# Kernel tuning notes

Measured on AMD Instinct MI355X. Metric: run time of the kernel, lower is better.

## Reference

```python
import jax, jax.numpy as jnp
import numpy as np

D_MODEL = 1024
N_HEADS = 16
HEAD_DIM = D_MODEL // N_HEADS  # 64
BATCH, SEQ = 2, 2048
MASK_FILL = -1000000000.0


def setup_inputs() -> dict:
    key = jax.random.key(0)
    ks = jax.random.split(key, 13)
    s = 1.0 / np.sqrt(D_MODEL)
    inp = {
        "q": jax.random.normal(ks[0], (BATCH, SEQ, D_MODEL), jnp.float32),
        "k": jax.random.normal(ks[1], (BATCH, SEQ, D_MODEL), jnp.float32),
        "v": jax.random.normal(ks[2], (BATCH, SEQ, D_MODEL), jnp.float32),
        "mask": jax.random.randint(ks[3], (BATCH, 1, SEQ, SEQ), 0, 2, jnp.int32),
        "Wq": jax.random.normal(ks[4], (D_MODEL, D_MODEL), jnp.float32) * s,
        "bq": jax.random.normal(ks[5], (D_MODEL,), jnp.float32) * s,
        "Wk": jax.random.normal(ks[6], (D_MODEL, D_MODEL), jnp.float32) * s,
        "bk": jax.random.normal(ks[7], (D_MODEL,), jnp.float32) * s,
        "Wv": jax.random.normal(ks[8], (D_MODEL, D_MODEL), jnp.float32) * s,
        "bv": jax.random.normal(ks[9], (D_MODEL,), jnp.float32) * s,
        "Wo": jax.random.normal(ks[10], (D_MODEL, D_MODEL), jnp.float32) * s,
        "bo": jax.random.normal(ks[11], (D_MODEL,), jnp.float32) * s,
    }
    return inp


def reference(q, k, v, mask, Wq, bq, Wk, bk, Wv, bv, Wo, bo):
    batch, seq, feat = q.shape
    # Linear projections (torch Linear: x @ W.T + b)
    qp = q @ Wq.T + bq
    kp = k @ Wk.T + bk
    vp = v @ Wv.T + bv

    def split(x):
        # (B, S, D) -> (B, H, S, Dh)
        return x.reshape(batch, seq, N_HEADS, HEAD_DIM).swapaxes(1, 2)

    qh, kh, vh = split(qp), split(kp), split(vp)

    # (B, H, S, S) score matrix, scaled
    score = jnp.einsum("bhqd,bhkd->bhqk", qh, kh) / jnp.sqrt(
        jnp.asarray(HEAD_DIM, qh.dtype))
    score = jnp.where(mask == 0, jnp.asarray(MASK_FILL, score.dtype), score)
    attn = jax.nn.softmax(score, axis=-1)
    out = jnp.einsum("bhqk,bhkd->bhqd", attn, vh)  # (B, H, S, Dh)
    joint = out.swapaxes(1, 2).reshape(batch, seq, feat)
    return joint @ Wo.T + bo
```

## Files before the change

kernel.cpp:

```cpp
#include <hip/hip_runtime.h>

typedef unsigned short u16;
typedef unsigned long long u64;
typedef float f32x4 __attribute__((ext_vector_type(4)));
typedef __bf16 bf16x4 __attribute__((ext_vector_type(4)));
typedef __bf16 bf16x8 __attribute__((ext_vector_type(8)));
typedef u16 u16x8 __attribute__((ext_vector_type(8)));

#define QSCALE 0.18033688011112042f

__device__ __forceinline__ u16 f2bf(float f) {
  unsigned int u = __float_as_uint(f);
  u += 0x7fffu + ((u >> 16) & 1u);
  return (u16)(u >> 16);
}

__device__ __forceinline__ void async16(const void* g, void* l) {
  __builtin_amdgcn_global_load_lds(
      (__attribute__((address_space(1))) void*)g,
      (__attribute__((address_space(3))) void*)l,
      16, 0, 0);
}

__device__ __forceinline__ f32x4 mfma16(bf16x8 a, bf16x8 b, f32x4 c) {
  return __builtin_amdgcn_mfma_f32_16x16x32_bf16(a, b, c, 0, 0, 0);
}

struct CvtArgs {
  const float* src[7];
  u16* dst[7];
};

__global__ __launch_bounds__(256) void cvt_kernel(CvtArgs a) {
  int z = blockIdx.z;
  int n = (z < 3) ? 4194304 : 1048576;
  int base = (blockIdx.x * 256 + threadIdx.x) * 8;
  if (base >= n) return;
  const float* s = a.src[z] + base;
  f32x4 x0 = *(const f32x4*)s;
  f32x4 x1 = *(const f32x4*)(s + 4);
  u16x8 pk;
  pk[0]=f2bf(x0[0]); pk[1]=f2bf(x0[1]); pk[2]=f2bf(x0[2]); pk[3]=f2bf(x0[3]);
  pk[4]=f2bf(x1[0]); pk[5]=f2bf(x1[1]); pk[6]=f2bf(x1[2]); pk[7]=f2bf(x1[3]);
  *(u16x8*)(a.dst[z] + base) = pk;
}

__global__ __launch_bounds__(256) void pack_mask_kernel(
    const int* __restrict__ mask, u64* __restrict__ pm) {
  int idx = blockIdx.x * 256 + threadIdx.x;
  const int4* src = (const int4*)(mask + (size_t)idx * 64);
  u64 bits = 0ull;
#pragma unroll
  for (int j = 0; j < 16; ++j) {
    int4 v = src[j];
    if (v.x) bits |= 1ull << (4 * j + 0);
    if (v.y) bits |= 1ull << (4 * j + 1);
    if (v.z) bits |= 1ull << (4 * j + 2);
    if (v.w) bits |= 1ull << (4 * j + 3);
  }
  pm[idx] = bits;
}

__device__ __forceinline__ void gemm_body(const u16* __restrict__ A,
                                          const u16* __restrict__ W,
                                          const float* __restrict__ bias,
                                          void* __restrict__ outraw, int mode,
                                          float oscale) {
  alignas(16) __shared__ u16 lA[128 * 32];
  alignas(16) __shared__ u16 lB[128 * 32];
  const int tid = threadIdx.x;
  const int lane = tid & 63, wv = tid >> 6;
  const int wm = wv >> 1, wn = wv & 1;
  const int m0 = blockIdx.y * 128, n0 = blockIdx.x * 128;
  const int l15 = lane & 15, quad = lane >> 4;
  const int srow = lane >> 2;
  const int scol = (lane & 3) * 8;

  f32x4 acc[4][4] = {};

  for (int k0 = 0; k0 < 1024; k0 += 32) {
#pragma unroll
    for (int t = 0; t < 2; ++t) {
      int rb = (wv * 2 + t) * 16;
      async16(A + (size_t)(m0 + rb + srow) * 1024 + k0 + scol, (char*)lA + rb * 64);
      async16(W + (size_t)(n0 + rb + srow) * 1024 + k0 + scol, (char*)lB + rb * 64);
    }
    __syncthreads();
    bf16x8 af[4], bfr[4];
#pragma unroll
    for (int i = 0; i < 4; ++i) {
      af[i]  = *(const bf16x8*)(lA + (wm * 64 + i * 16 + l15) * 32 + quad * 8);
      bfr[i] = *(const bf16x8*)(lB + (wn * 64 + i * 16 + l15) * 32 + quad * 8);
    }
#pragma unroll
    for (int i = 0; i < 4; ++i)
#pragma unroll
      for (int j = 0; j < 4; ++j)
        acc[i][j] = mfma16(af[i], bfr[j], acc[i][j]);
    __syncthreads();
  }

#pragma unroll
  for (int i = 0; i < 4; ++i) {
    int mbase = m0 + wm * 64 + i * 16 + quad * 4;
#pragma unroll
    for (int j = 0; j < 4; ++j) {
      int n = n0 + wn * 64 + j * 16 + l15;
      float bv = bias[n];
#pragma unroll
      for (int r = 0; r < 4; ++r) {
        int m = mbase + r;
        float val = (acc[i][j][r] + bv) * oscale;
        if (mode == 0) {
          int b = m >> 11, s = m & 2047, h = n >> 6, dh = n & 63;
          ((u16*)outraw)[((((size_t)b * 16 + h) * 2048 + s) << 6) + dh] = f2bf(val);
        } else if (mode == 1) {
          int b = m >> 11, s = m & 2047, h = n >> 6, dh = n & 63;
          ((u16*)outraw)[((((size_t)b * 16 + h) * 64 + dh) << 11) + s] = f2bf(val);
        } else {
          ((float*)outraw)[(size_t)m * 1024 + n] = val;
        }
      }
    }
  }
}

__global__ __launch_bounds__(256) void gemm_qkv_kernel(
    const u16* __restrict__ qb, const u16* __restrict__ kb, const u16* __restrict__ vb,
    const u16* __restrict__ Wqb, const float* __restrict__ bq,
    const u16* __restrict__ Wkb, const float* __restrict__ bk,
    const u16* __restrict__ Wvb, const float* __restrict__ bv,
    u16* __restrict__ qp, u16* __restrict__ kp, u16* __restrict__ vt) {
  if (blockIdx.z == 0)      gemm_body(qb, Wqb, bq, qp, 0, QSCALE);
  else if (blockIdx.z == 1) gemm_body(kb, Wkb, bk, kp, 0, 1.0f);
  else                      gemm_body(vb, Wvb, bv, vt, 1, 1.0f);
}

__global__ __launch_bounds__(256) void gemm_o_kernel(
    const u16* __restrict__ joint, const u16* __restrict__ Wob,
    const float* __restrict__ bo, float* __restrict__ out) {
  gemm_body(joint, Wob, bo, out, 2, 1.0f);
}

__global__ __launch_bounds__(256, 4) void attn_kernel(
    const u16* __restrict__ qp, const u16* __restrict__ kp,
    const u16* __restrict__ vt, const u64* __restrict__ pm,
    u16* __restrict__ joint) {
  alignas(16) __shared__ u16 kbuf[2][4096];
  alignas(16) __shared__ u16 vbuf[2][4096];
  alignas(16) __shared__ u16 pbuf[4][1024];

  const int tid = threadIdx.x, lane = tid & 63, wv = tid >> 6;
  const int quad = lane >> 4, l15 = lane & 15;
  const int q0 = blockIdx.x * 64;
  const int h = blockIdx.y, b = blockIdx.z;
  const size_t head_off = ((size_t)b * 16 + h) * 2048 * 64;
  const u16* Qh = qp + head_off;
  const u16* Kh = kp + head_off;
  const u16* Vh = vt + head_off;
  const int qr = q0 + wv * 16 + l15;
  const u64* pmq = pm + ((size_t)b * 2048 + qr) * 32;

  bf16x8 qf[2];
  {
    const u16* qrow = Qh + (size_t)qr * 64 + quad * 8;
    qf[0] = *(const bf16x8*)(qrow);
    qf[1] = *(const bf16x8*)(qrow + 32);
  }

  const int sd0 = tid, sd1 = 256 + tid;
  const int snt0 = sd0 >> 7, shalf0 = (sd0 >> 6) & 1, sl60 = sd0 & 63;
  const int snt1 = sd1 >> 7, shalf1 = (sd1 >> 6) & 1, sl61 = sd1 & 63;
  const u16* kg0 = Kh + (size_t)(snt0 * 16 + (sl60 & 15)) * 64 + shalf0 * 32 + (sl60 >> 4) * 8;
  const u16* kg1 = Kh + (size_t)(snt1 * 16 + (sl61 & 15)) * 64 + shalf1 * 32 + (sl61 >> 4) * 8;
  const int vb0 = sd0 >> 6, vb1 = sd1 >> 6;
  const u16* vg0 = Vh + (size_t)((vb0 >> 1) * 16 + (sl60 & 15)) * 2048 + (vb0 & 1) * 32 + (sl60 >> 4) * 8;
  const u16* vg1 = Vh + (size_t)((vb1 >> 1) * 16 + (sl61 & 15)) * 2048 + (vb1 & 1) * 32 + (sl61 >> 4) * 8;

  f32x4 O[4] = {};
  f32x4 lacc = {};
  const f32x4 fz = {};

  async16(kg0, (char*)kbuf[0] + sd0 * 16);
  async16(kg1, (char*)kbuf[0] + sd1 * 16);
  async16(vg0, (char*)vbuf[0] + sd0 * 16);
  async16(vg1, (char*)vbuf[0] + sd1 * 16);

  for (int kt = 0; kt < 32; ++kt) {
    __syncthreads();

    if (kt != 31) {
      const size_t kadv = (size_t)(kt + 1) * 4096;
      const int vadv = (kt + 1) * 64;
      char* kd = (char*)kbuf[(kt + 1) & 1];
      char* vd = (char*)vbuf[(kt + 1) & 1];
      async16(kg0 + kadv, kd + sd0 * 16);
      async16(kg1 + kadv, kd + sd1 * 16);
      async16(vg0 + vadv, vd + sd0 * 16);
      async16(vg1 + vadv, vd + sd1 * 16);
    }

    u64 word = pmq[kt];
    const u16* kc = kbuf[kt & 1];
    const u16* vc = vbuf[kt & 1];

    bf16x8 kf[8];
#pragma unroll
    for (int nt = 0; nt < 4; ++nt) {
      kf[2 * nt]     = *(const bf16x8*)(kc + nt * 1024 + lane * 8);
      kf[2 * nt + 1] = *(const bf16x8*)(kc + nt * 1024 + 512 + lane * 8);
    }

    f32x4 S[4];
#pragma unroll
    for (int nt = 0; nt < 4; ++nt) {
      f32x4 z = mfma16(kf[2 * nt], qf[0], fz);
      S[nt] = mfma16(kf[2 * nt + 1], qf[1], z);
    }

    {
      unsigned int wlo = (unsigned int)word, whi = (unsigned int)(word >> 32);
#pragma unroll
      for (int nt = 0; nt < 4; ++nt) {
        unsigned int hw = (nt < 2) ? wlo : whi;
        unsigned int nib = hw >> ((nt & 1) * 16 + quad * 4);
#pragma unroll
        for (int r = 0; r < 4; ++r) {
          float pe = __builtin_amdgcn_exp2f(S[nt][r]);
          S[nt][r] = ((nib >> r) & 1u) ? pe : 0.f;
        }
        lacc += S[nt];
        bf16x4 pv = __builtin_convertvector(S[nt], bf16x4);
        int t4 = 4 * nt + quad;
        int ks = t4 >> 3, qd = (t4 & 7) >> 1;
        u16* pw = pbuf[wv] + ks * 512 + qd * 128 + l15 * 8 + (t4 & 1) * 4;
        *(u64*)pw = *(const u64*)&pv;
      }
    }

    bf16x8 vf[8];
#pragma unroll
    for (int nt = 0; nt < 4; ++nt) {
      vf[2 * nt]     = *(const bf16x8*)(vc + (nt * 2) * 512 + lane * 8);
      vf[2 * nt + 1] = *(const bf16x8*)(vc + (nt * 2 + 1) * 512 + lane * 8);
    }
    asm volatile("s_waitcnt lgkmcnt(0)" ::: "memory");

#pragma unroll
    for (int ks = 0; ks < 2; ++ks) {
      bf16x8 pf = *(const bf16x8*)(pbuf[wv] + ks * 512 + lane * 8);
#pragma unroll
      for (int nt = 0; nt < 4; ++nt)
        O[nt] = mfma16(vf[2 * nt + ks], pf, O[nt]);
    }
  }

  {
    float l = (lacc[0] + lacc[1]) + (lacc[2] + lacc[3]);
    l += __shfl_xor(l, 16, 64);
    l += __shfl_xor(l, 32, 64);
    float inv = 1.0f / l;
    size_t row_off = ((size_t)b * 2048 + qr) * 1024 + h * 64;
#pragma unroll
    for (int nt = 0; nt < 4; ++nt) {
      f32x4 ov = O[nt] * inv;
      bf16x4 obv = __builtin_convertvector(ov, bf16x4);
      *(u64*)(joint + row_off + nt * 16 + quad * 4) = *(const u64*)&obv;
    }
  }
}

extern "C" void kernel_launch(void* const* d_in, const int* in_sizes, int n_in,
                              void* d_out, int out_size, void* d_ws, size_t ws_size,
                              hipStream_t stream) {
  const float* q  = (const float*)d_in[0];
  const float* k  = (const float*)d_in[1];
  const float* v  = (const float*)d_in[2];
  const int* mask = (const int*)d_in[3];
  const float* Wq = (const float*)d_in[4];
  const float* bq = (const float*)d_in[5];
  const float* Wk = (const float*)d_in[6];
  const float* bk = (const float*)d_in[7];
  const float* Wv = (const float*)d_in[8];
  const float* bv = (const float*)d_in[9];
  const float* Wo = (const float*)d_in[10];
  const float* bo = (const float*)d_in[11];
  float* out = (float*)d_out;

  u16* w = (u16*)d_ws;
  u16* qp    = w;
  u16* kp    = w + 4194304;
  u16* vt    = w + 8388608;
  u16* qb    = w + 12582912;
  u16* kb    = w + 16777216;
  u16* vb    = w + 20971520;
  u16* Wqb   = w + 25165824;
  u16* Wkb   = w + 26214400;
  u16* Wvb   = w + 27262976;
  u16* Wob   = w + 28311552;
  u64* pm    = (u64*)(w + 29360128);
  u16* joint = qb;

  CvtArgs ca;
  ca.src[0] = q;  ca.dst[0] = qb;
  ca.src[1] = k;  ca.dst[1] = kb;
  ca.src[2] = v;  ca.dst[2] = vb;
  ca.src[3] = Wq; ca.dst[3] = Wqb;
  ca.src[4] = Wk; ca.dst[4] = Wkb;
  ca.src[5] = Wv; ca.dst[5] = Wvb;
  ca.src[6] = Wo; ca.dst[6] = Wob;

  pack_mask_kernel<<<dim3(512), dim3(256), 0, stream>>>(mask, pm);
  cvt_kernel<<<dim3(2048, 1, 7), dim3(256), 0, stream>>>(ca);
  gemm_qkv_kernel<<<dim3(8, 32, 3), dim3(256), 0, stream>>>(
      qb, kb, vb, Wqb, bq, Wkb, bk, Wvb, bv, qp, kp, vt);
  attn_kernel<<<dim3(32, 16, 2), dim3(256), 0, stream>>>(qp, kp, vt, pm, joint);
  gemm_o_kernel<<<dim3(8, 32, 1), dim3(256), 0, stream>>>(joint, Wob, bo, out);
}
```

Measured before the change: 300.4 us.

## Rewrite attention with 32x32 MFMA, register-resident P and swizzled LDS

The attention kernel moves from 16x16x32 to 32x32x16 bf16 MFMA tiles, so each wave handles 32 query rows and each block handles 128 queries, halving the grid. Instead of staging P through a per-wave LDS buffer, the probabilities are packed to bf16 in registers and rearranged across lanes with permlane32 swaps to form the B operand directly. K/V tiles are loaded into LDS with an XOR swizzle to avoid bank conflicts. This removes the P round trip through LDS and its waitcnt, but it raises register pressure (launch bounds drop to 2 blocks per SM) and gives fewer blocks to spread across CUs.

```diff
diff --git a/kernel.cpp b/kernel.cpp
--- a/kernel.cpp
+++ b/kernel.cpp
@@ -1,11 +1,14 @@
 #include <hip/hip_runtime.h>
 
 typedef unsigned short u16;
+typedef unsigned int u32;
 typedef unsigned long long u64;
 typedef float f32x4 __attribute__((ext_vector_type(4)));
+typedef float f32x16 __attribute__((ext_vector_type(16)));
 typedef __bf16 bf16x4 __attribute__((ext_vector_type(4)));
 typedef __bf16 bf16x8 __attribute__((ext_vector_type(8)));
 typedef u16 u16x8 __attribute__((ext_vector_type(8)));
+typedef u32 u32x4 __attribute__((ext_vector_type(4)));
 
 #define QSCALE 0.18033688011112042f
 
@@ -24,6 +27,20 @@
 
 __device__ __forceinline__ f32x4 mfma16(bf16x8 a, bf16x8 b, f32x4 c) {
   return __builtin_amdgcn_mfma_f32_16x16x32_bf16(a, b, c, 0, 0, 0);
+}
+
+__device__ __forceinline__ f32x16 mfma32(bf16x8 a, bf16x8 b, f32x16 c) {
+  return __builtin_amdgcn_mfma_f32_32x32x16_bf16(a, b, c, 0, 0, 0);
+}
+
+__device__ __forceinline__ u32 cvtpk(float lo, float hi) {
+  u32 r;
+  asm("v_cvt_pk_bf16_f32 %0, %1, %2" : "=v"(r) : "v"(lo), "v"(hi));
+  return r;
+}
+
+__device__ __forceinline__ void pswap(u32& a, u32& b) {
+  asm("v_permlane32_swap_b32 %0, %1" : "+v"(a), "+v"(b));
 }
 
 struct CvtArgs {
@@ -142,44 +159,42 @@
   gemm_body(joint, Wob, bo, out, 2, 1.0f);
 }
 
-__global__ __launch_bounds__(256, 4) void attn_kernel(
+__global__ __launch_bounds__(256, 2) void attn_kernel(
     const u16* __restrict__ qp, const u16* __restrict__ kp,
     const u16* __restrict__ vt, const u64* __restrict__ pm,
     u16* __restrict__ joint) {
   alignas(16) __shared__ u16 kbuf[2][4096];
   alignas(16) __shared__ u16 vbuf[2][4096];
-  alignas(16) __shared__ u16 pbuf[4][1024];
 
   const int tid = threadIdx.x, lane = tid & 63, wv = tid >> 6;
-  const int quad = lane >> 4, l15 = lane & 15;
-  const int q0 = blockIdx.x * 64;
-  const int h = blockIdx.y, b = blockIdx.z;
-  const size_t head_off = ((size_t)b * 16 + h) * 2048 * 64;
+  const int l31 = lane & 31, hi = lane >> 5, l7 = lane & 7;
+  const int q0 = blockIdx.x * 128;
+  const int hd = blockIdx.y, b = blockIdx.z;
+  const size_t head_off = ((size_t)b * 16 + hd) * 2048 * 64;
   const u16* Qh = qp + head_off;
   const u16* Kh = kp + head_off;
   const u16* Vh = vt + head_off;
-  const int qr = q0 + wv * 16 + l15;
+  const int qr = q0 + wv * 32 + l31;
   const u64* pmq = pm + ((size_t)b * 2048 + qr) * 32;
 
-  bf16x8 qf[2];
+  bf16x8 qf[4];
   {
-    const u16* qrow = Qh + (size_t)qr * 64 + quad * 8;
-    qf[0] = *(const bf16x8*)(qrow);
-    qf[1] = *(const bf16x8*)(qrow + 32);
+    const u16* qrow = Qh + (size_t)qr * 64 + hi * 8;
+#pragma unroll
+    for (int d = 0; d < 4; ++d) qf[d] = *(const bf16x8*)(qrow + d * 16);
   }
 
   const int sd0 = tid, sd1 = 256 + tid;
-  const int snt0 = sd0 >> 7, shalf0 = (sd0 >> 6) & 1, sl60 = sd0 & 63;
-  const int snt1 = sd1 >> 7, shalf1 = (sd1 >> 6) & 1, sl61 = sd1 & 63;
-  const u16* kg0 = Kh + (size_t)(snt0 * 16 + (sl60 & 15)) * 64 + shalf0 * 32 + (sl60 >> 4) * 8;
-  const u16* kg1 = Kh + (size_t)(snt1 * 16 + (sl61 & 15)) * 64 + shalf1 * 32 + (sl61 >> 4) * 8;
-  const int vb0 = sd0 >> 6, vb1 = sd1 >> 6;
-  const u16* vg0 = Vh + (size_t)((vb0 >> 1) * 16 + (sl60 & 15)) * 2048 + (vb0 & 1) * 32 + (sl60 >> 4) * 8;
-  const u16* vg1 = Vh + (size_t)((vb1 >> 1) * 16 + (sl61 & 15)) * 2048 + (vb1 & 1) * 32 + (sl61 >> 4) * 8;
-
-  f32x4 O[4] = {};
+  const int kr0 = sd0 >> 3, ks0 = ((sd0 & 7) ^ (kr0 & 7)) * 8;
+  const int kr1 = sd1 >> 3, ks1 = ((sd1 & 7) ^ (kr1 & 7)) * 8;
+  const u16* kg0 = Kh + (size_t)kr0 * 64 + ks0;
+  const u16* kg1 = Kh + (size_t)kr1 * 64 + ks1;
+  const u16* vg0 = Vh + (size_t)kr0 * 2048 + ks0;
+  const u16* vg1 = Vh + (size_t)kr1 * 2048 + ks1;
+
+  f32x16 O[2] = {};
   f32x4 lacc = {};
-  const f32x4 fz = {};
+  const f32x16 fz16 = {};
 
   async16(kg0, (char*)kbuf[0] + sd0 * 16);
   async16(kg1, (char*)kbuf[0] + sd1 * 16);
@@ -201,72 +216,95 @@
     }
 
     u64 word = pmq[kt];
-    const u16* kc = kbuf[kt & 1];
-    const u16* vc = vbuf[kt & 1];
-
-    bf16x8 kf[8];
-#pragma unroll
-    for (int nt = 0; nt < 4; ++nt) {
-      kf[2 * nt]     = *(const bf16x8*)(kc + nt * 1024 + lane * 8);
-      kf[2 * nt + 1] = *(const bf16x8*)(kc + nt * 1024 + 512 + lane * 8);
-    }
-
-    f32x4 S[4];
-#pragma unroll
-    for (int nt = 0; nt < 4; ++nt) {
-      f32x4 z = mfma16(kf[2 * nt], qf[0], fz);
-      S[nt] = mfma16(kf[2 * nt + 1], qf[1], z);
-    }
+    const char* kc = (const char*)kbuf[kt & 1];
+    const char* vc = (const char*)vbuf[kt & 1];
+
+    bf16x8 kf[2][4];
+#pragma unroll
+    for (int h = 0; h < 2; ++h)
+#pragma unroll
+      for (int d = 0; d < 4; ++d)
+        kf[h][d] = *(const bf16x8*)(kc + (h * 32 + l31) * 128 +
+                                    (((2 * d + hi) ^ l7) << 4));
+
+    f32x16 S[2];
+#pragma unroll
+    for (int h = 0; h < 2; ++h) {
+      f32x16 s = mfma32(kf[h][0], qf[0], fz16);
+      s = mfma32(kf[h][1], qf[1], s);
+      s = mfma32(kf[h][2], qf[2], s);
+      S[h] = mfma32(kf[h][3], qf[3], s);
+    }
+
+    bf16x8 vf[2][4];
+#pragma unroll
+    for (int g = 0; g < 2; ++g)
+#pragma unroll
+      for (int ks = 0; ks < 4; ++ks)
+        vf[g][ks] = *(const bf16x8*)(vc + (g * 32 + l31) * 128 +
+                                     (((2 * ks + hi) ^ l7) << 4));
 
     {
-      unsigned int wlo = (unsigned int)word, whi = (unsigned int)(word >> 32);
-#pragma unroll
-      for (int nt = 0; nt < 4; ++nt) {
-        unsigned int hw = (nt < 2) ? wlo : whi;
-        unsigned int nib = hw >> ((nt & 1) * 16 + quad * 4);
-#pragma unroll
-        for (int r = 0; r < 4; ++r) {
-          float pe = __builtin_amdgcn_exp2f(S[nt][r]);
-          S[nt][r] = ((nib >> r) & 1u) ? pe : 0.f;
+      const int hi4 = hi * 4;
+#pragma unroll
+      for (int h = 0; h < 2; ++h) {
+        u32 wh = (h == 0) ? (u32)word : (u32)(word >> 32);
+#pragma unroll
+        for (int rq = 0; rq < 4; ++rq) {
+          u32 nib = wh >> (rq * 8 + hi4);
+#pragma unroll
+          for (int r4 = 0; r4 < 4; ++r4) {
+            int i = rq * 4 + r4;
+            float pe = __builtin_amdgcn_exp2f(S[h][i]);
+            S[h][i] = ((nib >> r4) & 1u) ? pe : 0.f;
+          }
+          f32x4 sv = {S[h][rq * 4 + 0], S[h][rq * 4 + 1],
+                      S[h][rq * 4 + 2], S[h][rq * 4 + 3]};
+          lacc += sv;
         }
-        lacc += S[nt];
-        bf16x4 pv = __builtin_convertvector(S[nt], bf16x4);
-        int t4 = 4 * nt + quad;
-        int ks = t4 >> 3, qd = (t4 & 7) >> 1;
-        u16* pw = pbuf[wv] + ks * 512 + qd * 128 + l15 * 8 + (t4 & 1) * 4;
-        *(u64*)pw = *(const u64*)&pv;
       }
     }
 
-    bf16x8 vf[8];
-#pragma unroll
-    for (int nt = 0; nt < 4; ++nt) {
-      vf[2 * nt]     = *(const bf16x8*)(vc + (nt * 2) * 512 + lane * 8);
-      vf[2 * nt + 1] = *(const bf16x8*)(vc + (nt * 2 + 1) * 512 + lane * 8);
-    }
-    asm volatile("s_waitcnt lgkmcnt(0)" ::: "memory");
-
-#pragma unroll
-    for (int ks = 0; ks < 2; ++ks) {
-      bf16x8 pf = *(const bf16x8*)(pbuf[wv] + ks * 512 + lane * 8);
-#pragma unroll
-      for (int nt = 0; nt < 4; ++nt)
-        O[nt] = mfma16(vf[2 * nt + ks], pf, O[nt]);
+    bf16x8 pf[4];
+#pragma unroll
+    for (int ks = 0; ks < 4; ++ks) {
+      int h = ks >> 1;
+      int ra = (ks & 1) * 8;
+      u32 w0a = cvtpk(S[h][ra + 0], S[h][ra + 1]);
+      u32 w1a = cvtpk(S[h][ra + 2], S[h][ra + 3]);
+      u32 w0b = cvtpk(S[h][ra + 4], S[h][ra + 5]);
+      u32 w1b = cvtpk(S[h][ra + 6], S[h][ra + 7]);
+      pswap(w0a, w0b);
+      pswap(w1a, w1b);
+      u32x4 t = {w0a, w1a, w0b, w1b};
+      pf[ks] = __builtin_bit_cast(bf16x8, t);
+    }
+
+#pragma unroll
+    for (int g = 0; g < 2; ++g) {
+      f32x16 o = O[g];
+      o = mfma32(vf[g][0], pf[0], o);
+      o = mfma32(vf[g][1], pf[1], o);
+      o = mfma32(vf[g][2], pf[2], o);
+      O[g] = mfma32(vf[g][3], pf[3], o);
     }
   }
 
   {
     float l = (lacc[0] + lacc[1]) + (lacc[2] + lacc[3]);
-    l += __shfl_xor(l, 16, 64);
     l += __shfl_xor(l, 32, 64);
     float inv = 1.0f / l;
-    size_t row_off = ((size_t)b * 2048 + qr) * 1024 + h * 64;
-#pragma unroll
-    for (int nt = 0; nt < 4; ++nt) {
-      f32x4 ov = O[nt] * inv;
-      bf16x4 obv = __builtin_convertvector(ov, bf16x4);
-      *(u64*)(joint + row_off + nt * 16 + quad * 4) = *(const u64*)&obv;
-    }
+    size_t row_off = ((size_t)b * 2048 + qr) * 1024 + hd * 64;
+#pragma unroll
+    for (int g = 0; g < 2; ++g)
+#pragma unroll
+      for (int rq = 0; rq < 4; ++rq) {
+        f32x4 ov = {O[g][rq * 4 + 0] * inv, O[g][rq * 4 + 1] * inv,
+                    O[g][rq * 4 + 2] * inv, O[g][rq * 4 + 3] * inv};
+        bf16x4 obv = __builtin_convertvector(ov, bf16x4);
+        *(u64*)(joint + row_off + g * 32 + rq * 8 + hi * 4) =
+            *(const u64*)&obv;
+      }
   }
 }
 
@@ -314,6 +352,6 @@
   cvt_kernel<<<dim3(2048, 1, 7), dim3(256), 0, stream>>>(ca);
   gemm_qkv_kernel<<<dim3(8, 32, 3), dim3(256), 0, stream>>>(
       qb, kb, vb, Wqb, bq, Wkb, bk, Wvb, bv, qp, kp, vt);
-  attn_kernel<<<dim3(32, 16, 2), dim3(256), 0, stream>>>(qp, kp, vt, pm, joint);
+  attn_kernel<<<dim3(16, 16, 2), dim3(256), 0, stream>>>(qp, kp, vt, pm, joint);
   gemm_o_kernel<<<dim3(8, 32, 1), dim3(256), 0, stream>>>(joint, Wob, bo, out);
 }
```

After: 286.1 us. 1.05x faster.
